# Kernel tuning notes

Measured on AMD Instinct MI355X. Metric: run time of the kernel, lower is better.

## Reference

```python
import math
import jax, jax.numpy as jnp
import numpy as np

DRAGON_ITERATIONS = 12
DRAGON_SMOOTHING = 0.1


def _dragon_patterns(iterations=DRAGON_ITERATIONS, smoothing=DRAGON_SMOOTHING):
    """Deterministic (non-learned) Dragon curve patterns, matching torch impl."""
    patterns = [np.array([0.5], dtype=np.float32)]
    kernel = np.ones(3, dtype=np.float32) / 3.0
    for _ in range(1, iterations):
        prev = patterns[-1]
        n = len(prev)
        newp = np.zeros(2 * n + 1, dtype=np.float32)
        newp[:n] = prev
        newp[n] = 0.5
        newp[n + 1:] = 1.0 - prev[::-1]
        if smoothing > 0:
            # conv1d with kernel_size=3, padding=1 (zero pad) == np.convolve 'same'
            newp = np.convolve(newp, kernel, mode='same').astype(np.float32)
        newp = (newp - newp.min()) / (newp.max() - newp.min() + 1e-8)
        patterns.append(newp.astype(np.float32))
    return patterns

_PATTERNS = _dragon_patterns()


def _interp_pattern(seq_len):
    """Linearly interpolate selected dragon pattern to seq_len (static shapes)."""
    it = min(int(math.log2(seq_len)), DRAGON_ITERATIONS - 1)
    pattern = _PATTERNS[it]
    if len(pattern) == seq_len:
        w = pattern.copy()
    else:
        x_old = np.linspace(0.0, 1.0, len(pattern), dtype=np.float64)
        x_new = np.linspace(0.0, 1.0, seq_len, dtype=np.float64)
        w = np.interp(x_new, x_old, pattern.astype(np.float64)).astype(np.float32)
    return it, jnp.asarray(w)


def setup_inputs() -> dict:
    key = jax.random.key(0)
    ks = jax.random.split(key, 8)
    B, S, D = 8, 2048, 512
    query = jax.random.normal(ks[0], (B, S, D), dtype=jnp.float32)
    k = jax.random.normal(ks[1], (B, S, D), dtype=jnp.float32)
    value = jax.random.normal(ks[2], (B, S, D), dtype=jnp.float32)
    pattern_scale = jnp.ones((DRAGON_ITERATIONS,), dtype=jnp.float32)
    pattern_bias = jnp.zeros((DRAGON_ITERATIONS,), dtype=jnp.float32)
    w1 = jax.random.normal(ks[3], (DRAGON_ITERATIONS, 64), dtype=jnp.float32) * (1.0 / math.sqrt(DRAGON_ITERATIONS))
    b1 = jnp.zeros((64,), dtype=jnp.float32)
    w2 = jax.random.normal(ks[4], (64, 1), dtype=jnp.float32) * (1.0 / 8.0)
    b2 = jnp.zeros((1,), dtype=jnp.float32)
    return {"query": query, "key": k, "value": value,
            "pattern_scale": pattern_scale, "pattern_bias": pattern_bias,
            "w1": w1, "b1": b1, "w2": w2, "b2": b2}


def reference(query, key, value, pattern_scale, pattern_bias, w1, b1, w2, b2):
    B, S, D = key.shape
    it, base_w = _interp_pattern(S)
    # learned affine + softplus on dragon weights
    dragon_w = jax.nn.softplus(base_w * pattern_scale[it] + pattern_bias[it])  # [S]
    weighted_keys = key * dragon_w[None, :, None]                              # [B,S,D]
    scores = jnp.einsum('bqd,bkd->bqk', query, weighted_keys) / math.sqrt(D)   # [B,S,S]
    attn = jax.nn.softmax(scores, axis=-1)
    # blend factor from one-hot iteration features through tiny MLP
    feat = jax.nn.one_hot(it, DRAGON_ITERATIONS, dtype=query.dtype)            # [12]
    h = jax.nn.relu(feat @ w1 + b1)
    blend = jax.nn.sigmoid(h @ w2 + b2)                                        # [1]
    blend = blend[0]
    final_attn = blend * attn + (1.0 - blend) / S                              # uniform blend
    out = jnp.einsum('bqk,bkd->bqd', final_attn, value)                        # [B,S,D]
    # original does output.squeeze(1); S>1 so it's a no-op here
    return out
```

## Files before the change

kernel.cpp:

```cpp
#include <hip/hip_runtime.h>
#include <cstdint>

#define DEV __device__ __forceinline__

typedef float f32x4 __attribute__((ext_vector_type(4)));
typedef short s16x8 __attribute__((ext_vector_type(8)));

DEV unsigned short f2bf(float f){
    unsigned u = __builtin_bit_cast(unsigned, f);
    u = u + 0x7fffu + ((u >> 16) & 1u);
    return (unsigned short)(u >> 16);
}
DEV float bf2f(unsigned short h){
    unsigned u = ((unsigned)h) << 16;
    return __builtin_bit_cast(float, u);
}

typedef const void __attribute__((address_space(1)))* gcp;
typedef void __attribute__((address_space(3)))* lp;
DEV void gload_lds16(const void* g, void* l){
    __builtin_amdgcn_global_load_lds((gcp)g, (lp)l, 16, 0, 0);
}

__global__ __launch_bounds__(256) void k_stage1(
    const float* __restrict__ Q, const float* __restrict__ K,
    const float* __restrict__ V,
    const float* __restrict__ scale, const float* __restrict__ bias,
    const float* __restrict__ w1, const float* __restrict__ b1,
    const float* __restrict__ w2, const float* __restrict__ b2,
    float* __restrict__ dragon_w, float* __restrict__ blend_out,
    unsigned short* __restrict__ Qb, unsigned short* __restrict__ Kb,
    unsigned short* __restrict__ Vt, float* __restrict__ vmean_part)
{
    __shared__ float sh[8704];
    int tid = threadIdx.x;
    int bx  = blockIdx.x;

    if (bx == 0){
        float* A    = sh;
        float* Bb   = sh + 4096;
        float* sred = sh + 8192;
        if (tid == 0) A[0] = 0.5f;
        __syncthreads();
        int len = 1;
        for (int it = 1; it < 12; ++it){
            int n = len, nl = 2*n + 1;
            for (int i = tid; i < nl; i += 256){
                float v;
                if (i < n)       v = A[i];
                else if (i == n) v = 0.5f;
                else             v = 1.0f - A[2*n - i];
                Bb[i] = v;
            }
            __syncthreads();
            const float third = 1.0f/3.0f;
            for (int i = tid; i < nl; i += 256){
                float s = Bb[i]*third;
                if (i > 0)    s += Bb[i-1]*third;
                if (i < nl-1) s += Bb[i+1]*third;
                A[i] = s;
            }
            __syncthreads();
            float mn = 3.4e38f, mx = -3.4e38f;
            for (int i = tid; i < nl; i += 256){ float v = A[i]; mn = fminf(mn,v); mx = fmaxf(mx,v); }
            sred[tid] = mn; sred[256 + tid] = mx;
            __syncthreads();
            for (int off = 128; off > 0; off >>= 1){
                if (tid < off){
                    sred[tid]       = fminf(sred[tid],       sred[tid+off]);
                    sred[256 + tid] = fmaxf(sred[256 + tid], sred[256 + tid + off]);
                }
                __syncthreads();
            }
            float lo = sred[0], den = sred[256] - lo + 1e-8f;
            for (int i = tid; i < nl; i += 256) A[i] = (A[i] - lo) / den;
            len = nl;
            __syncthreads();
        }
        float sc = scale[11], bi = bias[11];
        for (int i = tid; i < 2048; i += 256){
            float x = A[2*i]*sc + bi;
            dragon_w[i] = fmaxf(x, 0.f) + log1pf(__expf(-fabsf(x)));
        }
        if (tid < 64){
            float h = fmaxf(w1[11*64 + tid] + b1[tid], 0.f);
            float c = h * w2[tid];
            for (int off = 32; off > 0; off >>= 1) c += __shfl_xor(c, off, 64);
            if (tid == 0) blend_out[0] = 1.f/(1.f + __expf(-(c + b2[0])));
        }
        return;
    }

    if (bx <= 4096){
        const float* src = (bx <= 2048) ? Q : K;
        unsigned short* dst = (bx <= 2048) ? Qb : Kb;
        int bi = (bx <= 2048) ? (bx-1) : (bx-2049);
        const long long total4 = (long long)8*2048*512/4;
        long long stride = 2048LL*256;
        for (long long i = (long long)bi*256 + tid; i < total4; i += stride){
            long long base = i*4;
            const float4 q = *(const float4*)(src + base);
            ushort4 qo;
            qo.x = f2bf(q.x); qo.y = f2bf(q.y); qo.z = f2bf(q.z); qo.w = f2bf(q.w);
            *(ushort4*)(dst + base) = qo;
        }
        return;
    }

    int t = bx - 4097;
    int stile = t & 31, dtile = (t >> 5) & 7, b = t >> 8;
    int s0 = stile*64, d0 = dtile*64;
    float (*tile)[67] = (float(*)[67])sh;
    float* red = sh + 4288;
    int c4 = tid & 15, rr = tid >> 4;
    const float* src = V + ((long long)b*2048 + s0)*512 + d0;
    #pragma unroll
    for (int p = 0; p < 4; ++p){
        int row = p*16 + rr;
        const float4 v = *(const float4*)(src + (long long)row*512 + c4*4);
        tile[row][c4*4+0] = v.x; tile[row][c4*4+1] = v.y;
        tile[row][c4*4+2] = v.z; tile[row][c4*4+3] = v.w;
    }
    __syncthreads();
    unsigned short* dst = Vt + ((long long)b*512 + d0)*2048 + s0;
    #pragma unroll
    for (int p = 0; p < 4; ++p){
        int d = p*16 + rr;
        ushort4 o;
        o.x = f2bf(tile[c4*4+0][d]);
        o.y = f2bf(tile[c4*4+1][d]);
        o.z = f2bf(tile[c4*4+2][d]);
        o.w = f2bf(tile[c4*4+3][d]);
        *(ushort4*)(dst + (long long)d*2048 + c4*4) = o;
    }
    int dcol = tid & 63, sp = tid >> 6;
    float s = 0.f;
    #pragma unroll
    for (int ii = 0; ii < 16; ++ii) s += tile[sp*16 + ii][dcol];
    red[sp*64 + dcol] = s;
    __syncthreads();
    if (sp == 0){
        float tot = red[dcol] + red[64+dcol] + red[128+dcol] + red[192+dcol];
        vmean_part[stile*4096 + b*512 + d0 + dcol] = tot * (1.0f/2048.0f);
    }
}

#define SCALE_QK 0.04419417382415922f

__global__ __launch_bounds__(256) void k_gemm_qk(
    const unsigned short* __restrict__ Qb, const unsigned short* __restrict__ Kb,
    const float* __restrict__ dragon_w,
    unsigned short* __restrict__ Sp, float* __restrict__ lpart)
{
    __shared__ unsigned short A0[128*64], B0[128*64];
    __shared__ unsigned short A1[128*64], B1[128*64];
    int tid = threadIdx.x;
    int lane = tid & 63, wave = tid >> 6;
    int wm = wave >> 1, wn = wave & 1;
    int ln = lane & 15, q4 = lane >> 4;
    int sx = ln & 7;
    int lid = (blockIdx.x & 7)*256 + (blockIdx.x >> 3);
    int kb = lid & 15, qb = (lid >> 4) & 15, b = lid >> 8;
    int q0 = qb*128, k0 = kb*128;
    const unsigned short* Abase = Qb + ((long long)b*2048 + q0)*512;
    const unsigned short* Bbase = Kb + ((long long)b*2048 + k0)*512;

    f32x4 acc[4][4];
    #pragma unroll
    for (int i = 0; i < 4; ++i)
        #pragma unroll
        for (int j = 0; j < 4; ++j) acc[i][j] = (f32x4)0.0f;

    int cc = lane & 7;
    int rg = lane >> 3;

    auto STAGE = [&](unsigned short* dA, unsigned short* dB, int kt){
        #pragma unroll
        for (int c = 0; c < 4; ++c){
            int chunk = wave*4 + c;
            int row = chunk*8 + rg;
            int gc  = cc ^ (row & 7);
            gload_lds16(Abase + (long long)row*512 + kt*64 + gc*8, dA + chunk*512);
            gload_lds16(Bbase + (long long)row*512 + kt*64 + gc*8, dB + chunk*512);
        }
    };
    auto COMPUTE = [&](const unsigned short* At, const unsigned short* Bt){
        #pragma unroll
        for (int ks = 0; ks < 2; ++ks){
            s16x8 af[4], bfr[4];
            int cs = ((ks*4 + q4) ^ sx) * 8;
            #pragma unroll
            for (int i = 0; i < 4; ++i)
                af[i] = *(const s16x8*)&At[(wm*64 + i*16 + ln)*64 + cs];
            #pragma unroll
            for (int j = 0; j < 4; ++j)
                bfr[j] = *(const s16x8*)&Bt[(wn*64 + j*16 + ln)*64 + cs];
            #pragma unroll
            for (int i = 0; i < 4; ++i)
                #pragma unroll
                for (int j = 0; j < 4; ++j)
                    acc[i][j] = __builtin_amdgcn_mfma_f32_16x16x32_bf16(af[i], bfr[j], acc[i][j], 0, 0, 0);
        }
    };

    STAGE(A0, B0, 0); __syncthreads();
    STAGE(A1, B1, 1); COMPUTE(A0, B0); __syncthreads();
    STAGE(A0, B0, 2); COMPUTE(A1, B1); __syncthreads();
    STAGE(A1, B1, 3); COMPUTE(A0, B0); __syncthreads();
    STAGE(A0, B0, 4); COMPUTE(A1, B1); __syncthreads();
    STAGE(A1, B1, 5); COMPUTE(A0, B0); __syncthreads();
    STAGE(A0, B0, 6); COMPUTE(A1, B1); __syncthreads();
    STAGE(A1, B1, 7); COMPUTE(A0, B0); __syncthreads();
    COMPUTE(A1, B1); __syncthreads();

    float wj[4];
    #pragma unroll
    for (int j = 0; j < 4; ++j)
        wj[j] = dragon_w[k0 + wn*64 + j*16 + ln] * SCALE_QK;

    float* lred = (float*)A0;
    unsigned short* outp = Sp + (long long)b*2048*2048;
    #pragma unroll
    for (int i = 0; i < 4; ++i){
        float rs[4] = {0.f, 0.f, 0.f, 0.f};
        #pragma unroll
        for (int j = 0; j < 4; ++j){
            #pragma unroll
            for (int r = 0; r < 4; ++r){
                int q = q0 + wm*64 + i*16 + q4*4 + r;
                int k = k0 + wn*64 + j*16 + ln;
                float v = __expf(acc[i][j][r] * wj[j]);
                unsigned short h = f2bf(v);
                outp[(long long)q*2048 + k] = h;
                rs[r] += bf2f(h);
            }
        }
        #pragma unroll
        for (int r = 0; r < 4; ++r){
            float v = rs[r];
            v += __shfl_xor(v, 1, 16);
            v += __shfl_xor(v, 2, 16);
            v += __shfl_xor(v, 4, 16);
            v += __shfl_xor(v, 8, 16);
            if (ln == 0) lred[(wm*64 + i*16 + q4*4 + r)*2 + wn] = v;
        }
    }
    __syncthreads();
    if (tid < 128)
        lpart[((long long)b*16 + kb)*2048 + q0 + tid] = lred[tid*2] + lred[tid*2+1];
}

__global__ __launch_bounds__(256) void k_gemm_pv(
    const unsigned short* __restrict__ Sp, const unsigned short* __restrict__ Vt,
    const float* __restrict__ lpart, const float* __restrict__ vmean_part,
    const float* __restrict__ blendp, float* __restrict__ out)
{
    __shared__ unsigned short A0[128*64], B0[128*64];
    __shared__ unsigned short A1[128*64], B1[128*64];
    int tid = threadIdx.x;
    int lane = tid & 63, wave = tid >> 6;
    int wm = wave >> 1, wn = wave & 1;
    int ln = lane & 15, q4 = lane >> 4;
    int sx = ln & 7;
    int lid = (blockIdx.x & 7)*64 + (blockIdx.x >> 3);
    int db = lid & 3, qb = (lid >> 2) & 15, b = lid >> 6;
    int q0 = qb*128, d0 = db*128;
    const unsigned short* Abase = Sp + (long long)b*2048*2048 + (long long)q0*2048;
    const unsigned short* Bbase = Vt + ((long long)b*512 + d0)*2048;

    f32x4 acc[4][4];
    #pragma unroll
    for (int i = 0; i < 4; ++i)
        #pragma unroll
        for (int j = 0; j < 4; ++j) acc[i][j] = (f32x4)0.0f;

    int cc = lane & 7;
    int rg = lane >> 3;

    auto STAGE = [&](unsigned short* dA, unsigned short* dB, int kt){
        #pragma unroll
        for (int c = 0; c < 4; ++c){
            int chunk = wave*4 + c;
            int row = chunk*8 + rg;
            int gc  = cc ^ (row & 7);
            gload_lds16(Abase + (long long)row*2048 + kt*64 + gc*8, dA + chunk*512);
            gload_lds16(Bbase + (long long)row*2048 + kt*64 + gc*8, dB + chunk*512);
        }
    };
    auto COMPUTE = [&](const unsigned short* At, const unsigned short* Bt){
        #pragma unroll
        for (int ks = 0; ks < 2; ++ks){
            s16x8 af[4], bfr[4];
            int cs = ((ks*4 + q4) ^ sx) * 8;
            #pragma unroll
            for (int i = 0; i < 4; ++i)
                af[i] = *(const s16x8*)&At[(wm*64 + i*16 + ln)*64 + cs];
            #pragma unroll
            for (int j = 0; j < 4; ++j)
                bfr[j] = *(const s16x8*)&Bt[(wn*64 + j*16 + ln)*64 + cs];
            #pragma unroll
            for (int i = 0; i < 4; ++i)
                #pragma unroll
                for (int j = 0; j < 4; ++j)
                    acc[i][j] = __builtin_amdgcn_mfma_f32_16x16x32_bf16(af[i], bfr[j], acc[i][j], 0, 0, 0);
        }
    };

    STAGE(A0, B0, 0); __syncthreads();
    for (int kt = 0; kt < 16; ++kt){
        STAGE(A1, B1, 2*kt + 1);
        COMPUTE(A0, B0); __syncthreads();
        if (kt < 15) STAGE(A0, B0, 2*kt + 2);
        COMPUTE(A1, B1); __syncthreads();
    }

    float* l_sh  = (float*)A0;
    float* vm_sh = (float*)B0;
    if (tid < 128){
        float s = 0.f;
        #pragma unroll
        for (int kb = 0; kb < 16; ++kb)
            s += lpart[((long long)b*16 + kb)*2048 + q0 + tid];
        l_sh[tid] = 1.0f / s;
    } else {
        int d = tid - 128;
        float s = 0.f;
        #pragma unroll
        for (int st = 0; st < 32; ++st)
            s += vmean_part[st*4096 + b*512 + d0 + d];
        vm_sh[d] = s;
    }
    __syncthreads();

    float blend = blendp[0];
    float ib = 1.0f - blend;
    float* obase = out + ((long long)b*2048 + q0)*512 + d0;
    float vm[4];
    #pragma unroll
    for (int j = 0; j < 4; ++j) vm[j] = vm_sh[wn*64 + j*16 + ln];
    #pragma unroll
    for (int i = 0; i < 4; ++i){
        #pragma unroll
        for (int r = 0; r < 4; ++r){
            int ql = wm*64 + i*16 + q4*4 + r;
            float linv = l_sh[ql];
            #pragma unroll
            for (int j = 0; j < 4; ++j){
                int dl = wn*64 + j*16 + ln;
                obase[(long long)ql*512 + dl] = blend*acc[i][j][r]*linv + ib*vm[j];
            }
        }
    }
}

extern "C" void kernel_launch(void* const* d_in, const int* in_sizes, int n_in,
                              void* d_out, int out_size, void* d_ws, size_t ws_size,
                              hipStream_t stream)
{
    (void)in_sizes; (void)n_in; (void)out_size; (void)ws_size;
    const float* Q  = (const float*)d_in[0];
    const float* K  = (const float*)d_in[1];
    const float* V  = (const float*)d_in[2];
    const float* ps = (const float*)d_in[3];
    const float* pb = (const float*)d_in[4];
    const float* w1 = (const float*)d_in[5];
    const float* b1 = (const float*)d_in[6];
    const float* w2 = (const float*)d_in[7];
    const float* b2 = (const float*)d_in[8];
    float* out = (float*)d_out;

    char* ws = (char*)d_ws;
    float* dragon_w        = (float*)(ws);
    float* blend           = (float*)(ws + 8192);
    float* vmean_part      = (float*)(ws + 32768);
    size_t off = 32768 + (size_t)512*1024;
    unsigned short* Qb     = (unsigned short*)(ws + off);
    unsigned short* Kb     = (unsigned short*)(ws + off + (size_t)16*1024*1024);
    unsigned short* Vt     = (unsigned short*)(ws + off + (size_t)32*1024*1024);
    unsigned short* Sp     = (unsigned short*)(ws + off + (size_t)48*1024*1024);
    float* lpart           = (float*)(ws + off + (size_t)112*1024*1024);

    hipLaunchKernelGGL(k_stage1,  dim3(6145), dim3(256), 0, stream,
                       Q, K, V, ps, pb, w1, b1, w2, b2, dragon_w, blend,
                       Qb, Kb, Vt, vmean_part);
    hipLaunchKernelGGL(k_gemm_qk, dim3(2048), dim3(256), 0, stream,
                       Qb, Kb, dragon_w, Sp, lpart);
    hipLaunchKernelGGL(k_gemm_pv, dim3(512),  dim3(256), 0, stream,
                       Sp, Vt, lpart, vmean_part, blend, out);
}
```

Baseline: 239.2 us.

## Deepen GEMM prefetch with vmcnt-based waits, raise MFMA priority, single-wave dragon build

The two GEMM main loops now keep two stages in flight, waiting on vmcnt(8) plus a raw s_barrier instead of a full __syncthreads after each compute, so global-to-LDS loads overlap more with MFMA work. MFMA blocks are wrapped in s_setprio to favour the math waves. The dragon pattern build in block 0 runs in a single wave, using shuffle reductions and LDS fences in place of block-wide barriers. The wrap-around staging (tn modulo the tile count) issues redundant extra loads at the tail, and correctness depends on vmcnt counting matching the per-thread load count.

```diff
diff --git a/kernel.cpp b/kernel.cpp
--- a/kernel.cpp
+++ b/kernel.cpp
@@ -21,6 +21,10 @@
 DEV void gload_lds16(const void* g, void* l){
     __builtin_amdgcn_global_load_lds((gcp)g, (lp)l, 16, 0, 0);
 }
+
+DEV void bar(){ asm volatile("s_barrier" ::: "memory"); }
+#define WAIT_VM(n) asm volatile("s_waitcnt vmcnt(" #n ")" ::: "memory")
+#define LDSFENCE   asm volatile("s_waitcnt lgkmcnt(0)" ::: "memory")
 
 __global__ __launch_bounds__(256) void k_stage1(
     const float* __restrict__ Q, const float* __restrict__ K,
@@ -37,46 +41,43 @@
     int bx  = blockIdx.x;
 
     if (bx == 0){
-        float* A    = sh;
-        float* Bb   = sh + 4096;
-        float* sred = sh + 8192;
-        if (tid == 0) A[0] = 0.5f;
+        float* A  = sh;
+        float* Bb = sh + 4096;
+        if (tid < 64){
+            if (tid == 0) A[0] = 0.5f;
+            LDSFENCE;
+            int len = 1;
+            const float third = 1.0f/3.0f;
+            for (int it = 1; it < 12; ++it){
+                int n = len, nl = 2*n + 1;
+                for (int i = tid; i < nl; i += 64){
+                    float v;
+                    if (i < n)       v = A[i];
+                    else if (i == n) v = 0.5f;
+                    else             v = 1.0f - A[2*n - i];
+                    Bb[i] = v;
+                }
+                LDSFENCE;
+                float mn = 3.4e38f, mx = -3.4e38f;
+                for (int i = tid; i < nl; i += 64){
+                    float s = Bb[i]*third;
+                    if (i > 0)    s += Bb[i-1]*third;
+                    if (i < nl-1) s += Bb[i+1]*third;
+                    A[i] = s;
+                    mn = fminf(mn, s); mx = fmaxf(mx, s);
+                }
+                #pragma unroll
+                for (int off = 32; off > 0; off >>= 1){
+                    mn = fminf(mn, __shfl_xor(mn, off, 64));
+                    mx = fmaxf(mx, __shfl_xor(mx, off, 64));
+                }
+                float lo = mn, den = mx - lo + 1e-8f;
+                for (int i = tid; i < nl; i += 64) A[i] = (A[i] - lo) / den;
+                LDSFENCE;
+                len = nl;
+            }
+        }
         __syncthreads();
-        int len = 1;
-        for (int it = 1; it < 12; ++it){
-            int n = len, nl = 2*n + 1;
-            for (int i = tid; i < nl; i += 256){
-                float v;
-                if (i < n)       v = A[i];
-                else if (i == n) v = 0.5f;
-                else             v = 1.0f - A[2*n - i];
-                Bb[i] = v;
-            }
-            __syncthreads();
-            const float third = 1.0f/3.0f;
-            for (int i = tid; i < nl; i += 256){
-                float s = Bb[i]*third;
-                if (i > 0)    s += Bb[i-1]*third;
-                if (i < nl-1) s += Bb[i+1]*third;
-                A[i] = s;
-            }
-            __syncthreads();
-            float mn = 3.4e38f, mx = -3.4e38f;
-            for (int i = tid; i < nl; i += 256){ float v = A[i]; mn = fminf(mn,v); mx = fmaxf(mx,v); }
-            sred[tid] = mn; sred[256 + tid] = mx;
-            __syncthreads();
-            for (int off = 128; off > 0; off >>= 1){
-                if (tid < off){
-                    sred[tid]       = fminf(sred[tid],       sred[tid+off]);
-                    sred[256 + tid] = fmaxf(sred[256 + tid], sred[256 + tid + off]);
-                }
-                __syncthreads();
-            }
-            float lo = sred[0], den = sred[256] - lo + 1e-8f;
-            for (int i = tid; i < nl; i += 256) A[i] = (A[i] - lo) / den;
-            len = nl;
-            __syncthreads();
-        }
         float sc = scale[11], bi = bias[11];
         for (int i = tid; i < 2048; i += 256){
             float x = A[2*i]*sc + bi;
@@ -195,23 +196,29 @@
             #pragma unroll
             for (int j = 0; j < 4; ++j)
                 bfr[j] = *(const s16x8*)&Bt[(wn*64 + j*16 + ln)*64 + cs];
+            __builtin_amdgcn_s_setprio(1);
             #pragma unroll
             for (int i = 0; i < 4; ++i)
                 #pragma unroll
                 for (int j = 0; j < 4; ++j)
                     acc[i][j] = __builtin_amdgcn_mfma_f32_16x16x32_bf16(af[i], bfr[j], acc[i][j], 0, 0, 0);
+            __builtin_amdgcn_s_setprio(0);
         }
     };
 
-    STAGE(A0, B0, 0); __syncthreads();
-    STAGE(A1, B1, 1); COMPUTE(A0, B0); __syncthreads();
-    STAGE(A0, B0, 2); COMPUTE(A1, B1); __syncthreads();
-    STAGE(A1, B1, 3); COMPUTE(A0, B0); __syncthreads();
-    STAGE(A0, B0, 4); COMPUTE(A1, B1); __syncthreads();
-    STAGE(A1, B1, 5); COMPUTE(A0, B0); __syncthreads();
-    STAGE(A0, B0, 6); COMPUTE(A1, B1); __syncthreads();
-    STAGE(A1, B1, 7); COMPUTE(A0, B0); __syncthreads();
-    COMPUTE(A1, B1); __syncthreads();
+    STAGE(A0, B0, 0);
+    STAGE(A1, B1, 1);
+    WAIT_VM(8); bar();
+    #pragma unroll
+    for (int t = 0; t < 8; ++t){
+        if (t & 1) COMPUTE(A1, B1); else COMPUTE(A0, B0);
+        bar();
+        int tn = (t + 2) & 7;
+        if (t & 1) STAGE(A1, B1, tn); else STAGE(A0, B0, tn);
+        WAIT_VM(8);
+        bar();
+    }
+    WAIT_VM(0); bar();
 
     float wj[4];
     #pragma unroll
@@ -298,21 +305,28 @@
             #pragma unroll
             for (int j = 0; j < 4; ++j)
                 bfr[j] = *(const s16x8*)&Bt[(wn*64 + j*16 + ln)*64 + cs];
+            __builtin_amdgcn_s_setprio(1);
             #pragma unroll
             for (int i = 0; i < 4; ++i)
                 #pragma unroll
                 for (int j = 0; j < 4; ++j)
                     acc[i][j] = __builtin_amdgcn_mfma_f32_16x16x32_bf16(af[i], bfr[j], acc[i][j], 0, 0, 0);
+            __builtin_amdgcn_s_setprio(0);
         }
     };
 
-    STAGE(A0, B0, 0); __syncthreads();
-    for (int kt = 0; kt < 16; ++kt){
-        STAGE(A1, B1, 2*kt + 1);
-        COMPUTE(A0, B0); __syncthreads();
-        if (kt < 15) STAGE(A0, B0, 2*kt + 2);
-        COMPUTE(A1, B1); __syncthreads();
-    }
+    STAGE(A0, B0, 0);
+    STAGE(A1, B1, 1);
+    WAIT_VM(8); bar();
+    for (int t = 0; t < 32; ++t){
+        if (t & 1) COMPUTE(A1, B1); else COMPUTE(A0, B0);
+        bar();
+        int tn = (t + 2) & 31;
+        if (t & 1) STAGE(A1, B1, tn); else STAGE(A0, B0, tn);
+        WAIT_VM(8);
+        bar();
+    }
+    WAIT_VM(0); bar();
 
     float* l_sh  = (float*)A0;
     float* vm_sh = (float*)B0;
```

Result: no change. 243.6 us (+1.8%).
